# Kernel optimization log

Hardware: AMD Instinct MI355X
Metric: run time of the kernel (lower is better)

## Reference

```python
import jax, jax.numpy as jnp
import numpy as np

N_U = 50000; N_I = 50000; F = 128; H = 128; E = 800000; G = 512; C = 16; L = 3
EPS = 1e-5


def setup_inputs() -> dict:
    key = jax.random.key(0)
    ks = jax.random.split(key, 22)
    s = 1.0 / np.sqrt(H)
    inp = {}
    inp["x_user"] = jax.random.normal(ks[0], (N_U, F), jnp.float32)
    inp["x_item"] = jax.random.normal(ks[1], (N_I, F), jnp.float32)
    inp["edge_u2i"] = jnp.stack([jax.random.randint(ks[2], (E,), 0, N_U),
                                 jax.random.randint(ks[3], (E,), 0, N_I)])
    inp["edge_i2u"] = jnp.stack([jax.random.randint(ks[4], (E,), 0, N_I),
                                 jax.random.randint(ks[5], (E,), 0, N_U)])
    inp["batch_user"] = jnp.sort(jax.random.randint(ks[6], (N_U,), 0, G))
    inp["batch_item"] = jnp.sort(jax.random.randint(ks[7], (N_I,), 0, G))
    # GraphConv params per layer per relation (in-dim == hidden == 128, so stackable)
    inp["Wrel_u2i"] = jax.random.uniform(ks[8], (L, H, F), jnp.float32, -s, s)
    inp["Wroot_u2i"] = jax.random.uniform(ks[9], (L, H, F), jnp.float32, -s, s)
    inp["b_u2i"] = jax.random.uniform(ks[10], (L, H), jnp.float32, -s, s)
    inp["Wrel_i2u"] = jax.random.uniform(ks[11], (L, H, F), jnp.float32, -s, s)
    inp["Wroot_i2u"] = jax.random.uniform(ks[12], (L, H, F), jnp.float32, -s, s)
    inp["b_i2u"] = jax.random.uniform(ks[13], (L, H), jnp.float32, -s, s)
    # BatchNorm (one module per node type, reused across layers)
    inp["bn_g_user"] = jnp.ones((H,), jnp.float32)
    inp["bn_b_user"] = jnp.zeros((H,), jnp.float32)
    inp["bn_g_item"] = jnp.ones((H,), jnp.float32)
    inp["bn_b_item"] = jnp.zeros((H,), jnp.float32)
    # per-layer classifier heads
    inp["fc_W"] = jax.random.uniform(ks[14], (L, C, H), jnp.float32, -s, s)
    inp["fc_b"] = jax.random.uniform(ks[15], (L, C), jnp.float32, -s, s)
    return inp


def _graph_conv(x_src, x_dst, edge, Wrel, Wroot, b, n_dst):
    # GraphConv, aggr='add': W_rel @ sum_{j in N(i)} x_j + W_root @ x_i + b
    agg = jax.ops.segment_sum(x_src[edge[0]], edge[1], num_segments=n_dst)  # [n_dst, F]
    return agg @ Wrel.T + x_dst @ Wroot.T + b


def _bn(x, g, b):
    # BatchNorm1d over nodes, training-mode batch statistics (biased var)
    m = x.mean(0)
    v = jnp.mean((x - m) ** 2, axis=0)
    return (x - m) * jax.lax.rsqrt(v + EPS) * g + b


def reference(x_user, x_item, edge_u2i, edge_i2u, batch_user, batch_item,
              Wrel_u2i, Wroot_u2i, b_u2i, Wrel_i2u, Wroot_i2u, b_i2u,
              bn_g_user, bn_b_user, bn_g_item, bn_b_item, fc_W, fc_b):
    batch_all = jnp.concatenate([batch_user, batch_item])
    cnt = jax.ops.segment_sum(jnp.ones((N_U + N_I,), jnp.float32), batch_all,
                              num_segments=G)
    cnt = jnp.maximum(cnt, 1.0)[:, None]
    feats = []
    xu, xi = x_user, x_item
    for l in range(L):
        new_i = _graph_conv(xu, xi, edge_u2i, Wrel_u2i[l], Wroot_u2i[l], b_u2i[l], N_I)
        new_u = _graph_conv(xi, xu, edge_i2u, Wrel_i2u[l], Wroot_i2u[l], b_i2u[l], N_U)
        xu = _bn(jax.nn.relu(new_u), bn_g_user, bn_b_user)
        xi = _bn(jax.nn.relu(new_i), bn_g_item, bn_b_item)
        pooled = jax.ops.segment_sum(jnp.concatenate([xu, xi], 0), batch_all,
                                     num_segments=G) / cnt  # global mean pool [G, H]
        feats.append(pooled)
    feats = jnp.stack(feats)  # [L, G, H]
    # eval mode: F.dropout is identity; per-layer linear heads
    logits = jnp.einsum('lgh,lch->lgc', feats, fc_W) + fc_b[:, None, :]  # [L, G, C]
    return (logits, feats)
```

## Files before the change

kernel.cpp:

```cpp
#include <hip/hip_runtime.h>

#define NN 50000
#define FD 128
#define NE 800000
#define NG 512
#define NC 16
#define NL 3
#define NTOT 100000
#define NBLK 391
#define NBUCK 196
#define CAP 10240
#define BINTILE 2048
#define NBINBLK 782
#define BNEPS 1e-5f
#define LOGITS_N (NL*NG*NC)

typedef unsigned short u16;
typedef unsigned char u8;
typedef __attribute__((ext_vector_type(8))) short short8;
typedef __attribute__((ext_vector_type(4))) float f32x4;

#define OFF_GCNT     0ul
#define OFF_BCUR     4096ul
#define OFF_ACC      5120ul
#define MEMSET_BYTES 7168ul
#define OFF_USTART   7680ul
#define OFF_ISTART   10240ul
#define OFF_INVCNT   12800ul
#define OFF_BNSC     14848ul
#define OFF_BNSH     15872ul
#define OFF_ROWRANGE 16896ul
#define OFF_WB       817152ul
#define OFF_CSR      1210368ul
#define OFF_N0I      9238528ul
#define OFF_N0U      22038528ul
#define OFF_N1U      34838528ul
#define OFF_N1I      47638528ul
#define OFF_XU0      60438528ul
#define OFF_XI0      73238528ul
#define OFF_WBS      73238528ul
#define OFF_BVEC     73369600ul

static __device__ __forceinline__ float bf2f(u16 v) {
  return __uint_as_float(((unsigned)v) << 16);
}
static __device__ __forceinline__ u16 f2bf(float f) {
  unsigned u = __float_as_uint(f);
  return (u16)((u + 0x7FFFu + ((u >> 16) & 1u)) >> 16);
}
template<int RELU>
static __device__ __forceinline__ void accT8(float* a, int4 v) {
  unsigned w[4] = {(unsigned)v.x, (unsigned)v.y, (unsigned)v.z, (unsigned)v.w};
  #pragma unroll
  for (int i = 0; i < 4; i++) {
    float lo = __uint_as_float(w[i] << 16);
    float hi = __uint_as_float(w[i] & 0xffff0000u);
    if (RELU) { lo = lo > 0.f ? lo : 0.f; hi = hi > 0.f ? hi : 0.f; }
    a[2*i]   += lo;
    a[2*i+1] += hi;
  }
}
static __device__ __forceinline__ void unp8(float* a, int4 v) {
  a[0] = __uint_as_float(((unsigned)v.x) << 16);
  a[1] = __uint_as_float(((unsigned)v.x) & 0xffff0000u);
  a[2] = __uint_as_float(((unsigned)v.y) << 16);
  a[3] = __uint_as_float(((unsigned)v.y) & 0xffff0000u);
  a[4] = __uint_as_float(((unsigned)v.z) << 16);
  a[5] = __uint_as_float(((unsigned)v.z) & 0xffff0000u);
  a[6] = __uint_as_float(((unsigned)v.w) << 16);
  a[7] = __uint_as_float(((unsigned)v.w) & 0xffff0000u);
}
static __device__ __forceinline__ int relu2(int w) {
  int lo = (w & 0x00008000) ? 0 : (w & 0x0000FFFF);
  int hi = (w < 0)          ? 0 : (int)(w & 0xFFFF0000u);
  return lo | hi;
}

__global__ __launch_bounds__(256) void k_hist_batch(const int* __restrict__ bu,
                                                    const int* __restrict__ bi,
                                                    int* __restrict__ gcnt) {
  int i = blockIdx.x*256 + threadIdx.x;
  if (i >= NTOT) return;
  int type = i >= NN;
  int g = type ? bi[i-NN] : bu[i];
  atomicAdd(&gcnt[type*NG + g], 1);
}

__global__ __launch_bounds__(512) void k_scan_g(const int* __restrict__ gcnt,
                                                int* __restrict__ ustart,
                                                int* __restrict__ istart,
                                                float* __restrict__ invcnt) {
  __shared__ int pu[512], pi[512];
  int t = threadIdx.x;
  int cu = gcnt[t], ci = gcnt[NG + t];
  pu[t] = cu; pi[t] = ci;
  __syncthreads();
  for (int off = 1; off < 512; off <<= 1) {
    int vu = (t >= off) ? pu[t-off] : 0;
    int vi = (t >= off) ? pi[t-off] : 0;
    __syncthreads();
    pu[t] += vu; pi[t] += vi;
    __syncthreads();
  }
  ustart[t] = pu[t] - cu;
  istart[t] = pi[t] - ci;
  if (t == 511) { ustart[NG] = pu[511]; istart[NG] = pi[511]; }
  int c = cu + ci;
  invcnt[t] = 1.0f / (float)(c > 0 ? c : 1);
}

__global__ __launch_bounds__(256) void k_bin(const int* __restrict__ eu2i,
                                             const int* __restrict__ ei2u,
                                             int* __restrict__ bcursor,
                                             int* __restrict__ binned) {
  __shared__ int hist[256];
  __shared__ int scan[256];
  __shared__ int gbase[256];
  __shared__ int rbuf[BINTILE];
  __shared__ u8 rbk[BINTILE];
  int tid = threadIdx.x;
  int base = blockIdx.x * BINTILE;
  hist[tid] = 0;
  __syncthreads();
  int packr[8], bkr[8], rankr[8];
  #pragma unroll
  for (int c = 0; c < 8; c++) {
    int idx = base + c*256 + tid;
    if (idx < 2*NE) {
      int rel = idx >= NE;
      int e = rel ? idx - NE : idx;
      const int* edge = rel ? ei2u : eu2i;
      int s = edge[e];
      int d = edge[NE + e];
      int slot = d + (rel ? NN : 0);
      int bk = slot >> 9;
      bkr[c] = bk;
      packr[c] = ((slot & 511) << 17) | s;
      rankr[c] = atomicAdd(&hist[bk], 1);
    } else bkr[c] = -1;
  }
  __syncthreads();
  scan[tid] = hist[tid];
  __syncthreads();
  for (int o = 1; o < 256; o <<= 1) {
    int v = (tid >= o) ? scan[tid - o] : 0;
    __syncthreads();
    scan[tid] += v;
    __syncthreads();
  }
  if (tid < NBUCK && hist[tid] > 0)
    gbase[tid] = atomicAdd(&bcursor[tid], hist[tid]);
  __syncthreads();
  #pragma unroll
  for (int c = 0; c < 8; c++) {
    if (bkr[c] >= 0) {
      int bk = bkr[c];
      int lpos = scan[bk] - hist[bk] + rankr[c];
      rbuf[lpos] = packr[c];
      rbk[lpos] = (u8)bk;
    }
  }
  __syncthreads();
  int nv = min(BINTILE, 2*NE - base);
  for (int j = tid; j < nv; j += 256) {
    int bk = rbk[j];
    int outpos = bk*CAP + gbase[bk] + (j - (scan[bk] - hist[bk]));
    binned[outpos] = rbuf[j];
  }
}

__global__ __launch_bounds__(256) void k_csrbuild(const int* __restrict__ bcursor,
                                                  int* __restrict__ csrbin,
                                                  int2* __restrict__ rowrange) {
  __shared__ int lcnt[512];
  __shared__ int scan2[256];
  __shared__ int lcsr[CAP];
  int b = blockIdx.x;
  int tid = threadIdx.x;
  int slot0 = b << 9;
  int nslots = min(512, NTOT - slot0);
  int n = bcursor[b];
  int gb = b * CAP;
  lcnt[tid] = 0; lcnt[tid + 256] = 0;
  __syncthreads();
  for (int i = tid; i < n; i += 256) {
    int e = csrbin[gb + i];
    atomicAdd(&lcnt[e >> 17], 1);
  }
  __syncthreads();
  int v0 = lcnt[2*tid], v1 = lcnt[2*tid + 1];
  int ps = v0 + v1;
  scan2[tid] = ps;
  __syncthreads();
  for (int o = 1; o < 256; o <<= 1) {
    int v = (tid >= o) ? scan2[tid - o] : 0;
    __syncthreads();
    scan2[tid] += v;
    __syncthreads();
  }
  int e0 = scan2[tid] - ps;
  int e1 = e0 + v0;
  if (2*tid < nslots)     rowrange[slot0 + 2*tid]     = make_int2(gb + e0, gb + e0 + v0);
  if (2*tid + 1 < nslots) rowrange[slot0 + 2*tid + 1] = make_int2(gb + e1, gb + e1 + v1);
  __syncthreads();
  lcnt[2*tid] = e0; lcnt[2*tid + 1] = e1;
  __syncthreads();
  for (int i = tid; i < n; i += 256) {
    int e = csrbin[gb + i];
    int pos = atomicAdd(&lcnt[e >> 17], 1);
    lcsr[pos] = e & 0x1FFFF;
  }
  __syncthreads();
  for (int i = tid; i < n; i += 256) csrbin[gb + i] = lcsr[i];
}

__global__ __launch_bounds__(256) void k_castX(const float* __restrict__ xu,
                                               const float* __restrict__ xi,
                                               u16* __restrict__ xbu,
                                               u16* __restrict__ xbi) {
  int b = blockIdx.x;
  int half = b >= 6250;
  const float* src = half ? xi : xu;
  u16* dst = half ? xbi : xbu;
  int i = ((half ? b - 6250 : b)*256 + threadIdx.x) * 4;
  float4 v = *(const float4*)(src + i);
  ushort4 o = { f2bf(v.x), f2bf(v.y), f2bf(v.z), f2bf(v.w) };
  *(ushort4*)(dst + i) = o;
}

__global__ __launch_bounds__(256) void k_castW(const float* __restrict__ WrelA,
                                               const float* __restrict__ WrootA,
                                               const float* __restrict__ WrelB,
                                               const float* __restrict__ WrootB,
                                               u16* __restrict__ WB) {
  int idx = blockIdx.x*256 + threadIdx.x;
  int lr = idx >> 15;
  int rem = idx & 32767;
  int h = rem >> 8;
  int k = rem & 255;
  int l = lr >> 1;
  int rel = lr & 1;
  const float* Wr = rel ? WrelB : WrelA;
  const float* Wo = rel ? WrootB : WrootA;
  float v = (k < FD) ? Wr[(l*FD + h)*FD + k] : Wo[(l*FD + h)*FD + (k-FD)];
  WB[idx] = f2bf(v);
}

__global__ __launch_bounds__(256) void k_bnfold2(const float* __restrict__ WrelA,
                                                 const float* __restrict__ WrootA,
                                                 const float* __restrict__ WrelB,
                                                 const float* __restrict__ WrootB,
                                                 int l,
                                                 const float* __restrict__ accSQ,
                                                 const float* __restrict__ gu,
                                                 const float* __restrict__ bu_,
                                                 const float* __restrict__ gi,
                                                 const float* __restrict__ bi_,
                                                 u16* __restrict__ WBs,
                                                 float* __restrict__ bvec,
                                                 float* __restrict__ bnsc,
                                                 float* __restrict__ bnsh) {
  __shared__ float sc_l[256], sh_l[256];
  int tid = threadIdx.x;
  {
    int type = tid >> 7;
    int c = tid & 127;
    float s = accSQ[tid];
    float q = accSQ[256 + tid];
    float inv = 1.0f / (float)NN;
    float mean = s * inv;
    float var = q * inv - mean*mean;
    float rstd = rsqrtf(var + BNEPS);
    float g = type ? gi[c] : gu[c];
    float bb = type ? bi_[c] : bu_[c];
    float sc = rstd * g;
    sc_l[tid] = sc;
    sh_l[tid] = bb - mean * sc;
  }
  __syncthreads();
  int b = blockIdx.x;
  int lastb = gridDim.x - 1;
  if (b == lastb) {
    bnsc[tid] = sc_l[tid];
    bnsh[tid] = sh_l[tid];
  } else if (b < 64) {
    int e = b*256 + tid;
    int rel = e >> 13;
    int rem = e & 8191;
    int h = rem >> 6;
    int k0 = (rem & 63) * 4;
    const float* Wr = rel ? WrelB : WrelA;
    const float* Wo = rel ? WrootB : WrootA;
    const float* scs = sc_l + (rel ? 128 : 0);
    const float* scd = sc_l + (rel ? 0 : 128);
    u16 t[4];
    #pragma unroll
    for (int j = 0; j < 4; j++) {
      int k = k0 + j;
      float v = (k < FD) ? Wr[((size_t)l*FD + h)*FD + k] * scs[k]
                         : Wo[((size_t)l*FD + h)*FD + (k - FD)] * scd[k - FD];
      t[j] = f2bf(v);
    }
    ushort4 o = { t[0], t[1], t[2], t[3] };
    *(ushort4*)(WBs + rel*32768 + h*256 + k0) = o;
  } else {
    int vid = (b - 64)*256 + tid;
    int kind = vid >> 8;
    int rel = (vid >> 7) & 1;
    int h = vid & 127;
    const float* W = kind ? (rel ? WrootB : WrootA) : (rel ? WrelB : WrelA);
    const float* sh = sh_l + ((kind ^ rel) ? 128 : 0);
    const float* wrow = W + ((size_t)l*FD + h)*FD;
    float s = 0.f;
    #pragma unroll
    for (int k = 0; k < FD; k += 4) {
      float4 wv = *(const float4*)(wrow + k);
      float4 sv = { sh[k], sh[k+1], sh[k+2], sh[k+3] };
      s += wv.x*sv.x + wv.y*sv.y + wv.z*sv.z + wv.w*sv.w;
    }
    bvec[kind*256 + rel*128 + h] = s;
  }
}

template<int RELU>
__global__ __launch_bounds__(256) void k_gather(const u16* __restrict__ curU,
                                                const u16* __restrict__ curI,
                                                const int2* __restrict__ rowrange,
                                                const int* __restrict__ csr,
                                                u16* __restrict__ aggI,
                                                u16* __restrict__ aggU) {
  int b = blockIdx.x;
  int half = b >= 12500;
  int blk = half ? b - 12500 : b;
  const u16* src = half ? curI : curU;
  u16* out = half ? aggU : aggI;
  int slotbase = half ? NN : 0;
  int wid = __builtin_amdgcn_readfirstlane(threadIdx.x >> 6);
  int row = blk*4 + wid;
  int lane = threadIdx.x & 63;
  int q = lane >> 4;
  int c16 = (lane & 15) * 8;
  const u16* sp = src + c16;
  int2 pr = rowrange[slotbase + row];
  int p = pr.x, pe = pr.y;
  float a0[8], a1[8];
  #pragma unroll
  for (int j = 0; j < 8; j++) { a0[j] = 0.f; a1[j] = 0.f; }
  if (p + 8 <= pe) {
    int i0 = csr[p + q], i1 = csr[p + 4 + q];
    while (p + 16 <= pe) {
      int n0 = csr[p + 8 + q], n1 = csr[p + 12 + q];
      int4 v0 = *(const int4*)(sp + (size_t)i0*FD);
      int4 v1 = *(const int4*)(sp + (size_t)i1*FD);
      accT8<RELU>(a0, v0); accT8<RELU>(a1, v1);
      i0 = n0; i1 = n1; p += 8;
    }
    int4 v0 = *(const int4*)(sp + (size_t)i0*FD);
    int4 v1 = *(const int4*)(sp + (size_t)i1*FD);
    accT8<RELU>(a0, v0); accT8<RELU>(a1, v1);
    p += 8;
  }
  int rem = pe - p;
  if (q < rem) {
    int s = csr[p + q];
    accT8<RELU>(a0, *(const int4*)(sp + (size_t)s*FD));
  }
  if (q + 4 < rem) {
    int s = csr[p + 4 + q];
    accT8<RELU>(a1, *(const int4*)(sp + (size_t)s*FD));
  }
  #pragma unroll
  for (int j = 0; j < 8; j++) a0[j] += a1[j];
  #pragma unroll
  for (int j = 0; j < 8; j++) {
    a0[j] += __shfl_xor(a0[j], 16);
    a0[j] += __shfl_xor(a0[j], 32);
  }
  if (q == 0) {
    int4 o;
    o.x = (unsigned)f2bf(a0[0]) | ((unsigned)f2bf(a0[1]) << 16);
    o.y = (unsigned)f2bf(a0[2]) | ((unsigned)f2bf(a0[3]) << 16);
    o.z = (unsigned)f2bf(a0[4]) | ((unsigned)f2bf(a0[5]) << 16);
    o.w = (unsigned)f2bf(a0[6]) | ((unsigned)f2bf(a0[7]) << 16);
    *(int4*)(out + (size_t)row*FD + c16) = o;
  }
}

__global__ __launch_bounds__(256) void k_gemm(u16* __restrict__ newU,
                                              u16* __restrict__ newI,
                                              const u16* __restrict__ curU,
                                              const u16* __restrict__ curI,
                                              const u16* __restrict__ WBl,
                                              const float* __restrict__ bI2U,
                                              const float* __restrict__ bU2I,
                                              float* __restrict__ accSQ,
                                              const float* __restrict__ bvec,
                                              const int2* __restrict__ rowrange,
                                              int fold) {
  __shared__ u16 smem[128*72*2];
  __shared__ float Sred[2][4][128];
  u16* As = smem;
  u16* Bs = smem + 128*72;
  u16* Cs = smem;
  int ty = blockIdx.y;
  u16* A1 = ty ? newI : newU;
  const u16* A2 = ty ? curI : curU;
  const u16* WBp = ty ? WBl : (WBl + 32768);
  const float* bias = ty ? bU2I : bI2U;
  const float* b1p = bvec + (ty ? 0 : 128);
  const float* b2p = bvec + 256 + (ty ? 0 : 128);
  int slot0 = ty ? 0 : NN;
  int tid = threadIdx.x;
  int n0 = blockIdx.x * 128;
  int w = __builtin_amdgcn_readfirstlane(tid >> 6);
  int lane = tid & 63;
  int l15 = lane & 15;
  int quad = lane >> 4;
  f32x4 acc[2][8];
  #pragma unroll
  for (int tr = 0; tr < 2; tr++)
    #pragma unroll
    for (int tc = 0; tc < 8; tc++)
      acc[tr][tc] = (f32x4){0.f,0.f,0.f,0.f};

  for (int ch = 0; ch < 4; ch++) {
    const u16* Ap = (ch < 2) ? ((const u16*)A1 + ch*64) : (A2 + (ch-2)*64);
    int dorelu = fold && (ch >= 2);
    #pragma unroll
    for (int i = 0; i < 4; i++) {
      int e = i*256 + tid;
      int r = e >> 3, seg = e & 7;
      int4 v = {0,0,0,0};
      int gr = n0 + r;
      if (gr < NN) v = *(const int4*)(Ap + (size_t)gr*FD + seg*8);
      if (dorelu) { v.x = relu2(v.x); v.y = relu2(v.y); v.z = relu2(v.z); v.w = relu2(v.w); }
      *(int4*)&As[r*72 + seg*8] = v;
    }
    #pragma unroll
    for (int i = 0; i < 4; i++) {
      int e = i*256 + tid;
      int r = e >> 3, seg = e & 7;
      int4 v = *(const int4*)(WBp + r*256 + ch*64 + seg*8);
      *(int4*)&Bs[r*72 + seg*8] = v;
    }
    __syncthreads();
    #pragma unroll
    for (int ks = 0; ks < 2; ks++) {
      int kb = ks*32 + quad*8;
      short8 af0 = *(const short8*)&As[(w*32 + l15)*72 + kb];
      short8 af1 = *(const short8*)&As[(w*32 + 16 + l15)*72 + kb];
      short8 bf[8];
      #pragma unroll
      for (int tc = 0; tc < 8; tc++)
        bf[tc] = *(const short8*)&Bs[(tc*16 + l15)*72 + kb];
      #pragma unroll
      for (int tc = 0; tc < 8; tc++) {
        acc[0][tc] = __builtin_amdgcn_mfma_f32_16x16x32_bf16(af0, bf[tc], acc[0][tc], 0, 0, 0);
        acc[1][tc] = __builtin_amdgcn_mfma_f32_16x16x32_bf16(af1, bf[tc], acc[1][tc], 0, 0, 0);
      }
    }
    __syncthreads();
  }
  float sv[8], qv[8], bj[8], b1j[8];
  #pragma unroll
  for (int tc = 0; tc < 8; tc++) {
    int col = tc*16 + l15;
    float base = bias[col];
    if (fold) { base += b2p[col]; b1j[tc] = b1p[col]; } else b1j[tc] = 0.f;
    bj[tc] = base;
    sv[tc] = 0.f; qv[tc] = 0.f;
  }
  float dg[2][4] = {{0.f,0.f,0.f,0.f},{0.f,0.f,0.f,0.f}};
  if (fold) {
    #pragma unroll
    for (int tr = 0; tr < 2; tr++)
      #pragma unroll
      for (int gq = 0; gq < 4; gq++) {
        int r = n0 + w*32 + tr*16 + quad*4 + gq;
        if (r < NN) {
          int2 rr = rowrange[slot0 + r];
          dg[tr][gq] = (float)(rr.y - rr.x);
        }
      }
  }
  #pragma unroll
  for (int tr = 0; tr < 2; tr++) {
    int rl0 = w*32 + tr*16 + quad*4;
    int rbase = n0 + rl0;
    #pragma unroll
    for (int tc = 0; tc < 8; tc++) {
      int col = tc*16 + l15;
      #pragma unroll
      for (int g = 0; g < 4; g++) {
        int r = rbase + g;
        float v = acc[tr][tc][g] + bj[tc] + dg[tr][g]*b1j[tc];
        Cs[(rl0 + g)*132 + col] = f2bf(v);
        if (r < NN) {
          float y = v > 0.f ? v : 0.f;
          sv[tc] += y; qv[tc] += y*y;
        }
      }
    }
  }
  #pragma unroll
  for (int tc = 0; tc < 8; tc++) {
    sv[tc] += __shfl_xor(sv[tc], 16); qv[tc] += __shfl_xor(qv[tc], 16);
    sv[tc] += __shfl_xor(sv[tc], 32); qv[tc] += __shfl_xor(qv[tc], 32);
  }
  if (quad == 0) {
    #pragma unroll
    for (int tc = 0; tc < 8; tc++) {
      Sred[0][w][tc*16 + l15] = sv[tc];
      Sred[1][w][tc*16 + l15] = qv[tc];
    }
  }
  __syncthreads();
  if (tid < 128) {
    float s = Sred[0][0][tid] + Sred[0][1][tid] + Sred[0][2][tid] + Sred[0][3][tid];
    float q = Sred[1][0][tid] + Sred[1][1][tid] + Sred[1][2][tid] + Sred[1][3][tid];
    atomicAdd(&accSQ[ty*128 + tid], s);
    atomicAdd(&accSQ[256 + ty*128 + tid], q);
  }
  int prow = tid >> 4;
  int pc = (tid & 15) * 8;
  #pragma unroll
  for (int j = 0; j < 8; j++) {
    int row = j*16 + prow;
    int gr = n0 + row;
    int4 vv = *(const int4*)&Cs[row*132 + pc];
    if (gr < NN) *(int4*)(A1 + (size_t)gr*FD + pc) = vv;
  }
}

__global__ __launch_bounds__(256) void k_pool(const u16* __restrict__ newU,
                                              const u16* __restrict__ newI,
                                              const int* __restrict__ ustart,
                                              const int* __restrict__ istart,
                                              const float* __restrict__ bnsc,
                                              const float* __restrict__ bnsh,
                                              const float* __restrict__ invcnt,
                                              float* __restrict__ feats,
                                              float* __restrict__ accSQ) {
  __shared__ float red[16][128];
  int tid = threadIdx.x;
  int g = blockIdx.x;
  if (g == 0) { accSQ[tid] = 0.f; accSQ[256 + tid] = 0.f; }
  int rt = tid >> 4;
  int c8 = (tid & 15) * 8;
  float tot[8];
  #pragma unroll
  for (int j = 0; j < 8; j++) tot[j] = 0.f;
  #pragma unroll
  for (int type = 0; type < 2; type++) {
    const u16* in = type ? newI : newU;
    const int* st = type ? istart : ustart;
    int rs = st[g], re = st[g+1];
    float acc[8];
    #pragma unroll
    for (int j = 0; j < 8; j++) acc[j] = 0.f;
    int r = rs + rt;
    for (; r + 16 < re; r += 32) {
      int4 v0 = *(const int4*)(in + (size_t)r*FD + c8);
      int4 v1 = *(const int4*)(in + (size_t)(r+16)*FD + c8);
      float f0[8], f1[8];
      unp8(f0, v0); unp8(f1, v1);
      #pragma unroll
      for (int j = 0; j < 8; j++)
        acc[j] += (f0[j] > 0.f ? f0[j] : 0.f) + (f1[j] > 0.f ? f1[j] : 0.f);
    }
    for (; r < re; r += 16) {
      int4 v0 = *(const int4*)(in + (size_t)r*FD + c8);
      float f0[8];
      unp8(f0, v0);
      #pragma unroll
      for (int j = 0; j < 8; j++) acc[j] += f0[j] > 0.f ? f0[j] : 0.f;
    }
    #pragma unroll
    for (int j = 0; j < 8; j++) tot[j] += acc[j] * bnsc[type*128 + c8 + j];
    if (rt == 0) {
      float cnt = (float)(re - rs);
      #pragma unroll
      for (int j = 0; j < 8; j++) tot[j] += cnt * bnsh[type*128 + c8 + j];
    }
  }
  #pragma unroll
  for (int j = 0; j < 8; j++) red[rt][c8 + j] = tot[j];
  __syncthreads();
  if (tid < 128) {
    float s = 0.f;
    #pragma unroll
    for (int i = 0; i < 16; i++) s += red[i][tid];
    feats[(size_t)g*FD + tid] = s * invcnt[g];
  }
}

__global__ __launch_bounds__(256) void k_heads(const float* __restrict__ feats,
                                               const float* __restrict__ fcW,
                                               const float* __restrict__ fcb,
                                               float* __restrict__ logits) {
  int idx = blockIdx.x*256 + threadIdx.x;
  if (idx >= LOGITS_N) return;
  int l = idx >> 13;
  int rem = idx & 8191;
  int g = rem >> 4;
  int c = rem & 15;
  const float* f = feats + ((size_t)l*NG + g)*FD;
  const float* w = fcW + ((size_t)l*NC + c)*FD;
  float s = 0.f;
  #pragma unroll
  for (int k = 0; k < FD; k += 4) {
    float4 fv = *(const float4*)(f + k);
    float4 wv = *(const float4*)(w + k);
    s += fv.x*wv.x + fv.y*wv.y + fv.z*wv.z + fv.w*wv.w;
  }
  logits[idx] = s + fcb[l*NC + c];
}

extern "C" void kernel_launch(void* const* d_in, const int* in_sizes, int n_in,
                              void* d_out, int out_size, void* d_ws, size_t ws_size,
                              hipStream_t stream) {
  const float* x_user   = (const float*)d_in[0];
  const float* x_item   = (const float*)d_in[1];
  const int*   eu2i     = (const int*)d_in[2];
  const int*   ei2u     = (const int*)d_in[3];
  const int*   bu       = (const int*)d_in[4];
  const int*   bi       = (const int*)d_in[5];
  const float* Wrel_u2i = (const float*)d_in[6];
  const float* Wroot_u2i= (const float*)d_in[7];
  const float* b_u2i    = (const float*)d_in[8];
  const float* Wrel_i2u = (const float*)d_in[9];
  const float* Wroot_i2u= (const float*)d_in[10];
  const float* b_i2u    = (const float*)d_in[11];
  const float* bn_g_user= (const float*)d_in[12];
  const float* bn_b_user= (const float*)d_in[13];
  const float* bn_g_item= (const float*)d_in[14];
  const float* bn_b_item= (const float*)d_in[15];
  const float* fcW      = (const float*)d_in[16];
  const float* fcb      = (const float*)d_in[17];

  char* ws = (char*)d_ws;
  int*   gcnt   = (int*)(ws + OFF_GCNT);
  int*   bcursor= (int*)(ws + OFF_BCUR);
  float* accSQ  = (float*)(ws + OFF_ACC);
  int*   ustart = (int*)(ws + OFF_USTART);
  int*   istart = (int*)(ws + OFF_ISTART);
  float* invcnt = (float*)(ws + OFF_INVCNT);
  float* bnsc   = (float*)(ws + OFF_BNSC);
  float* bnsh   = (float*)(ws + OFF_BNSH);
  int2*  rowrange = (int2*)(ws + OFF_ROWRANGE);
  u16*   WB     = (u16*)(ws + OFF_WB);
  int*   csrbin = (int*)(ws + OFF_CSR);
  u16*   n0I    = (u16*)(ws + OFF_N0I);
  u16*   n0U    = (u16*)(ws + OFF_N0U);
  u16*   n1U    = (u16*)(ws + OFF_N1U);
  u16*   n1I    = (u16*)(ws + OFF_N1I);
  u16*   xu0    = (u16*)(ws + OFF_XU0);
  u16*   xi0    = (u16*)(ws + OFF_XI0);
  u16*   WBs    = (u16*)(ws + OFF_WBS);
  float* bvec   = (float*)(ws + OFF_BVEC);
  float* fout   = (float*)d_out;
  float* featsAll = fout + LOGITS_N;

  hipMemsetAsync(ws, 0, MEMSET_BYTES, stream);
  k_hist_batch<<<NBLK, 256, 0, stream>>>(bu, bi, gcnt);
  k_bin<<<NBINBLK, 256, 0, stream>>>(eu2i, ei2u, bcursor, csrbin);
  k_scan_g<<<1, 512, 0, stream>>>(gcnt, ustart, istart, invcnt);
  k_csrbuild<<<NBUCK, 256, 0, stream>>>(bcursor, csrbin, rowrange);
  k_castX<<<12500, 256, 0, stream>>>(x_user, x_item, xu0, xi0);
  k_castW<<<256, 256, 0, stream>>>(Wrel_u2i, Wroot_u2i, Wrel_i2u, Wroot_i2u, WB);

  k_gather<0><<<25000, 256, 0, stream>>>(xu0, xi0, rowrange, csrbin, n0I, n0U);
  k_gemm<<<dim3(NBLK,2), 256, 0, stream>>>(n0U, n0I, xu0, xi0, WB,
                                           b_i2u, b_u2i, accSQ,
                                           bvec, rowrange, 0);
  k_bnfold2<<<67, 256, 0, stream>>>(Wrel_u2i, Wroot_u2i, Wrel_i2u, Wroot_i2u,
                                    1, accSQ, bn_g_user, bn_b_user,
                                    bn_g_item, bn_b_item, WBs, bvec, bnsc, bnsh);
  k_pool<<<NG, 256, 0, stream>>>(n0U, n0I, ustart, istart, bnsc, bnsh,
                                 invcnt, featsAll, accSQ);

  k_gather<1><<<25000, 256, 0, stream>>>(n0U, n0I, rowrange, csrbin, n1I, n1U);
  k_gemm<<<dim3(NBLK,2), 256, 0, stream>>>(n1U, n1I, n0U, n0I, WBs,
                                           b_i2u + FD, b_u2i + FD, accSQ,
                                           bvec, rowrange, 1);
  k_bnfold2<<<67, 256, 0, stream>>>(Wrel_u2i, Wroot_u2i, Wrel_i2u, Wroot_i2u,
                                    2, accSQ, bn_g_user, bn_b_user,
                                    bn_g_item, bn_b_item, WBs, bvec, bnsc, bnsh);
  k_pool<<<NG, 256, 0, stream>>>(n1U, n1I, ustart, istart, bnsc, bnsh,
                                 invcnt, featsAll + NG*FD, accSQ);

  k_gather<1><<<25000, 256, 0, stream>>>(n1U, n1I, rowrange, csrbin, n0I, n0U);
  k_gemm<<<dim3(NBLK,2), 256, 0, stream>>>(n0U, n0I, n1U, n1I, WBs,
                                           b_i2u + 2*FD, b_u2i + 2*FD, accSQ,
                                           bvec, rowrange, 1);
  k_bnfold2<<<1, 256, 0, stream>>>(Wrel_u2i, Wroot_u2i, Wrel_i2u, Wroot_i2u,
                                   2, accSQ, bn_g_user, bn_b_user,
                                   bn_g_item, bn_b_item, WBs, bvec, bnsc, bnsh);
  k_pool<<<NG, 256, 0, stream>>>(n0U, n0I, ustart, istart, bnsc, bnsh,
                                 invcnt, featsAll + 2*NG*FD, accSQ);

  k_heads<<<96, 256, 0, stream>>>(featsAll, fcW, fcb, fout);
}
```

Measured before the change: 521.9 us.

## Fuse mean pooling into GEMM epilogue and merge preprocessing kernels

Removes the separate k_pool pass that re-read the new node features per graph. The GEMM epilogue now accumulates relu outputs per graph into a float P buffer, using shared-memory atomics for the first six graphs of a tile and global atomics otherwise. k_bnfold2 then applies the BN scale and shift to those pooled sums to produce feats. The cast-X, cast-W and batch-histogram kernels are merged into one k_pre launch, and double-banked stat accumulators replace zeroing in k_pool. The cost is extra atomics in the GEMM epilogue, and the float atomic sums make results order-dependent.

```diff
diff --git a/kernel.cpp b/kernel.cpp
--- a/kernel.cpp
+++ b/kernel.cpp
@@ -23,23 +23,20 @@
 #define OFF_GCNT     0ul
 #define OFF_BCUR     4096ul
 #define OFF_ACC      5120ul
-#define MEMSET_BYTES 7168ul
-#define OFF_USTART   7680ul
-#define OFF_ISTART   10240ul
-#define OFF_INVCNT   12800ul
-#define OFF_BNSC     14848ul
-#define OFF_BNSH     15872ul
+#define MEMSET_BYTES 9216ul
+#define OFF_USTART   9728ul
+#define OFF_ISTART   12288ul
+#define OFF_INVCNT   14848ul
 #define OFF_ROWRANGE 16896ul
 #define OFF_WB       817152ul
 #define OFF_CSR      1210368ul
 #define OFF_N0I      9238528ul
 #define OFF_N0U      22038528ul
-#define OFF_N1U      34838528ul
-#define OFF_N1I      47638528ul
+#define OFF_P        34838528ul
+#define OFF_WBS      35362816ul
+#define OFF_BVEC     35493888ul
 #define OFF_XU0      60438528ul
 #define OFF_XI0      73238528ul
-#define OFF_WBS      73238528ul
-#define OFF_BVEC     73369600ul
 
 static __device__ __forceinline__ float bf2f(u16 v) {
   return __uint_as_float(((unsigned)v) << 16);
@@ -60,30 +57,51 @@
     a[2*i+1] += hi;
   }
 }
-static __device__ __forceinline__ void unp8(float* a, int4 v) {
-  a[0] = __uint_as_float(((unsigned)v.x) << 16);
-  a[1] = __uint_as_float(((unsigned)v.x) & 0xffff0000u);
-  a[2] = __uint_as_float(((unsigned)v.y) << 16);
-  a[3] = __uint_as_float(((unsigned)v.y) & 0xffff0000u);
-  a[4] = __uint_as_float(((unsigned)v.z) << 16);
-  a[5] = __uint_as_float(((unsigned)v.z) & 0xffff0000u);
-  a[6] = __uint_as_float(((unsigned)v.w) << 16);
-  a[7] = __uint_as_float(((unsigned)v.w) & 0xffff0000u);
-}
 static __device__ __forceinline__ int relu2(int w) {
   int lo = (w & 0x00008000) ? 0 : (w & 0x0000FFFF);
   int hi = (w < 0)          ? 0 : (int)(w & 0xFFFF0000u);
   return lo | hi;
 }
 
-__global__ __launch_bounds__(256) void k_hist_batch(const int* __restrict__ bu,
-                                                    const int* __restrict__ bi,
-                                                    int* __restrict__ gcnt) {
-  int i = blockIdx.x*256 + threadIdx.x;
-  if (i >= NTOT) return;
-  int type = i >= NN;
-  int g = type ? bi[i-NN] : bu[i];
-  atomicAdd(&gcnt[type*NG + g], 1);
+__global__ __launch_bounds__(256) void k_pre(const float* __restrict__ xu,
+                                             const float* __restrict__ xi,
+                                             u16* __restrict__ xbu,
+                                             u16* __restrict__ xbi,
+                                             const float* __restrict__ WrelA,
+                                             const float* __restrict__ WrootA,
+                                             const float* __restrict__ WrelB,
+                                             const float* __restrict__ WrootB,
+                                             u16* __restrict__ WB,
+                                             const int* __restrict__ bu,
+                                             const int* __restrict__ bi,
+                                             int* __restrict__ gcnt) {
+  int b = blockIdx.x;
+  if (b < 12500) {
+    int half = b >= 6250;
+    const float* src = half ? xi : xu;
+    u16* dst = half ? xbi : xbu;
+    int i = ((half ? b - 6250 : b)*256 + threadIdx.x) * 4;
+    float4 v = *(const float4*)(src + i);
+    ushort4 o = { f2bf(v.x), f2bf(v.y), f2bf(v.z), f2bf(v.w) };
+    *(ushort4*)(dst + i) = o;
+  } else if (b < 12756) {
+    int idx = (b - 12500)*256 + threadIdx.x;
+    int lr = idx >> 15;
+    int rem = idx & 32767;
+    int h = rem >> 8;
+    int k = rem & 255;
+    int rel = lr & 1;
+    const float* Wr = rel ? WrelB : WrelA;
+    const float* Wo = rel ? WrootB : WrootA;
+    float v = (k < FD) ? Wr[h*FD + k] : Wo[h*FD + (k-FD)];
+    WB[idx] = f2bf(v);
+  } else {
+    int i = (b - 12756)*256 + threadIdx.x;
+    if (i >= NTOT) return;
+    int type = i >= NN;
+    int g = type ? bi[i-NN] : bu[i];
+    atomicAdd(&gcnt[type*NG + g], 1);
+  }
 }
 
 __global__ __launch_bounds__(512) void k_scan_g(const int* __restrict__ gcnt,
@@ -214,52 +232,25 @@
   for (int i = tid; i < n; i += 256) csrbin[gb + i] = lcsr[i];
 }
 
-__global__ __launch_bounds__(256) void k_castX(const float* __restrict__ xu,
-                                               const float* __restrict__ xi,
-                                               u16* __restrict__ xbu,
-                                               u16* __restrict__ xbi) {
-  int b = blockIdx.x;
-  int half = b >= 6250;
-  const float* src = half ? xi : xu;
-  u16* dst = half ? xbi : xbu;
-  int i = ((half ? b - 6250 : b)*256 + threadIdx.x) * 4;
-  float4 v = *(const float4*)(src + i);
-  ushort4 o = { f2bf(v.x), f2bf(v.y), f2bf(v.z), f2bf(v.w) };
-  *(ushort4*)(dst + i) = o;
-}
-
-__global__ __launch_bounds__(256) void k_castW(const float* __restrict__ WrelA,
-                                               const float* __restrict__ WrootA,
-                                               const float* __restrict__ WrelB,
-                                               const float* __restrict__ WrootB,
-                                               u16* __restrict__ WB) {
-  int idx = blockIdx.x*256 + threadIdx.x;
-  int lr = idx >> 15;
-  int rem = idx & 32767;
-  int h = rem >> 8;
-  int k = rem & 255;
-  int l = lr >> 1;
-  int rel = lr & 1;
-  const float* Wr = rel ? WrelB : WrelA;
-  const float* Wo = rel ? WrootB : WrootA;
-  float v = (k < FD) ? Wr[(l*FD + h)*FD + k] : Wo[(l*FD + h)*FD + (k-FD)];
-  WB[idx] = f2bf(v);
-}
-
 __global__ __launch_bounds__(256) void k_bnfold2(const float* __restrict__ WrelA,
                                                  const float* __restrict__ WrootA,
                                                  const float* __restrict__ WrelB,
                                                  const float* __restrict__ WrootB,
                                                  int l,
                                                  const float* __restrict__ accSQ,
+                                                 float* __restrict__ accSQz,
                                                  const float* __restrict__ gu,
                                                  const float* __restrict__ bu_,
-                                                 const float* __restrict__ gi,
+                                                 const float* __restrict__ gi_,
                                                  const float* __restrict__ bi_,
                                                  u16* __restrict__ WBs,
                                                  float* __restrict__ bvec,
-                                                 float* __restrict__ bnsc,
-                                                 float* __restrict__ bnsh) {
+                                                 float* __restrict__ P,
+                                                 const int* __restrict__ ustart,
+                                                 const int* __restrict__ istart,
+                                                 const float* __restrict__ invcnt,
+                                                 float* __restrict__ feats,
+                                                 int mode) {
   __shared__ float sc_l[256], sh_l[256];
   int tid = threadIdx.x;
   {
@@ -271,7 +262,7 @@
     float mean = s * inv;
     float var = q * inv - mean*mean;
     float rstd = rsqrtf(var + BNEPS);
-    float g = type ? gi[c] : gu[c];
+    float g = type ? gi_[c] : gu[c];
     float bb = type ? bi_[c] : bu_[c];
     float sc = rstd * g;
     sc_l[tid] = sc;
@@ -279,46 +270,59 @@
   }
   __syncthreads();
   int b = blockIdx.x;
-  int lastb = gridDim.x - 1;
-  if (b == lastb) {
-    bnsc[tid] = sc_l[tid];
-    bnsh[tid] = sh_l[tid];
-  } else if (b < 64) {
-    int e = b*256 + tid;
-    int rel = e >> 13;
-    int rem = e & 8191;
-    int h = rem >> 6;
-    int k0 = (rem & 63) * 4;
-    const float* Wr = rel ? WrelB : WrelA;
-    const float* Wo = rel ? WrootB : WrootA;
-    const float* scs = sc_l + (rel ? 128 : 0);
-    const float* scd = sc_l + (rel ? 0 : 128);
-    u16 t[4];
-    #pragma unroll
-    for (int j = 0; j < 4; j++) {
-      int k = k0 + j;
-      float v = (k < FD) ? Wr[((size_t)l*FD + h)*FD + k] * scs[k]
-                         : Wo[((size_t)l*FD + h)*FD + (k - FD)] * scd[k - FD];
-      t[j] = f2bf(v);
-    }
-    ushort4 o = { t[0], t[1], t[2], t[3] };
-    *(ushort4*)(WBs + rel*32768 + h*256 + k0) = o;
+  int nfold = mode ? 0 : 66;
+  if (b < nfold) {
+    if (b < 64) {
+      int e = b*256 + tid;
+      int rel = e >> 13;
+      int rem = e & 8191;
+      int h = rem >> 6;
+      int k0 = (rem & 63) * 4;
+      const float* Wr = rel ? WrelB : WrelA;
+      const float* Wo = rel ? WrootB : WrootA;
+      const float* scs = sc_l + (rel ? 128 : 0);
+      const float* scd = sc_l + (rel ? 0 : 128);
+      u16 t[4];
+      #pragma unroll
+      for (int j = 0; j < 4; j++) {
+        int k = k0 + j;
+        float v = (k < FD) ? Wr[((size_t)l*FD + h)*FD + k] * scs[k]
+                           : Wo[((size_t)l*FD + h)*FD + (k - FD)] * scd[k - FD];
+        t[j] = f2bf(v);
+      }
+      ushort4 o = { t[0], t[1], t[2], t[3] };
+      *(ushort4*)(WBs + rel*32768 + h*256 + k0) = o;
+    } else {
+      int vid = (b - 64)*256 + tid;
+      int kind = vid >> 8;
+      int rel = (vid >> 7) & 1;
+      int h = vid & 127;
+      const float* W = kind ? (rel ? WrootB : WrootA) : (rel ? WrelB : WrelA);
+      const float* sh = sh_l + ((kind ^ rel) ? 128 : 0);
+      const float* wrow = W + ((size_t)l*FD + h)*FD;
+      float s = 0.f;
+      #pragma unroll
+      for (int k = 0; k < FD; k += 4) {
+        float4 wv = *(const float4*)(wrow + k);
+        float4 sv = { sh[k], sh[k+1], sh[k+2], sh[k+3] };
+        s += wv.x*sv.x + wv.y*sv.y + wv.z*sv.z + wv.w*sv.w;
+      }
+      bvec[kind*256 + rel*128 + h] = s;
+    }
   } else {
-    int vid = (b - 64)*256 + tid;
-    int kind = vid >> 8;
-    int rel = (vid >> 7) & 1;
-    int h = vid & 127;
-    const float* W = kind ? (rel ? WrootB : WrootA) : (rel ? WrelB : WrelA);
-    const float* sh = sh_l + ((kind ^ rel) ? 128 : 0);
-    const float* wrow = W + ((size_t)l*FD + h)*FD;
-    float s = 0.f;
-    #pragma unroll
-    for (int k = 0; k < FD; k += 4) {
-      float4 wv = *(const float4*)(wrow + k);
-      float4 sv = { sh[k], sh[k+1], sh[k+2], sh[k+3] };
-      s += wv.x*sv.x + wv.y*sv.y + wv.z*sv.z + wv.w*sv.w;
-    }
-    bvec[kind*256 + rel*128 + h] = s;
+    int fb = b - nfold;
+    if (fb == 0) { accSQz[tid] = 0.f; accSQz[256 + tid] = 0.f; }
+    int g = fb*2 + (tid >> 7);
+    int ch = tid & 127;
+    size_t iu = (size_t)g*FD + ch;
+    size_t ii = (size_t)NG*FD + iu;
+    float pu = P[iu];
+    float pi = P[ii];
+    float cu = (float)(ustart[g+1] - ustart[g]);
+    float ci = (float)(istart[g+1] - istart[g]);
+    feats[iu] = invcnt[g] * (sc_l[ch]*pu + cu*sh_l[ch]
+                           + sc_l[128+ch]*pi + ci*sh_l[128+ch]);
+    P[iu] = 0.f; P[ii] = 0.f;
   }
 }
 
@@ -396,12 +400,16 @@
                                               float* __restrict__ accSQ,
                                               const float* __restrict__ bvec,
                                               const int2* __restrict__ rowrange,
+                                              const int* __restrict__ bu,
+                                              const int* __restrict__ bi,
+                                              float* __restrict__ P,
                                               int fold) {
   __shared__ u16 smem[128*72*2];
   __shared__ float Sred[2][4][128];
   u16* As = smem;
   u16* Bs = smem + 128*72;
   u16* Cs = smem;
+  float* Pl = (float*)&smem[16896];
   int ty = blockIdx.y;
   u16* A1 = ty ? newI : newU;
   const u16* A2 = ty ? curI : curU;
@@ -409,6 +417,8 @@
   const float* bias = ty ? bU2I : bI2U;
   const float* b1p = bvec + (ty ? 0 : 128);
   const float* b2p = bvec + 256 + (ty ? 0 : 128);
+  const int* batch = ty ? bi : bu;
+  float* Pg = P + (size_t)ty*NG*FD;
   int slot0 = ty ? 0 : NN;
   int tid = threadIdx.x;
   int n0 = blockIdx.x * 128;
@@ -461,6 +471,11 @@
     }
     __syncthreads();
   }
+  #pragma unroll
+  for (int i = 0; i < 3; i++) Pl[i*256 + tid] = 0.f;
+  __syncthreads();
+
+  int g0 = batch[n0];
   float sv[8], qv[8], bj[8], b1j[8];
   #pragma unroll
   for (int tc = 0; tc < 8; tc++) {
@@ -471,33 +486,37 @@
     sv[tc] = 0.f; qv[tc] = 0.f;
   }
   float dg[2][4] = {{0.f,0.f,0.f,0.f},{0.f,0.f,0.f,0.f}};
-  if (fold) {
-    #pragma unroll
-    for (int tr = 0; tr < 2; tr++)
-      #pragma unroll
-      for (int gq = 0; gq < 4; gq++) {
-        int r = n0 + w*32 + tr*16 + quad*4 + gq;
-        if (r < NN) {
+  int gix[2][4];
+  #pragma unroll
+  for (int tr = 0; tr < 2; tr++)
+    #pragma unroll
+    for (int gq = 0; gq < 4; gq++) {
+      int r = n0 + w*32 + tr*16 + quad*4 + gq;
+      gix[tr][gq] = -1;
+      if (r < NN) {
+        gix[tr][gq] = batch[r] - g0;
+        if (fold) {
           int2 rr = rowrange[slot0 + r];
           dg[tr][gq] = (float)(rr.y - rr.x);
         }
       }
-  }
+    }
   #pragma unroll
   for (int tr = 0; tr < 2; tr++) {
     int rl0 = w*32 + tr*16 + quad*4;
-    int rbase = n0 + rl0;
     #pragma unroll
     for (int tc = 0; tc < 8; tc++) {
       int col = tc*16 + l15;
       #pragma unroll
       for (int g = 0; g < 4; g++) {
-        int r = rbase + g;
         float v = acc[tr][tc][g] + bj[tc] + dg[tr][g]*b1j[tc];
         Cs[(rl0 + g)*132 + col] = f2bf(v);
-        if (r < NN) {
+        int gx = gix[tr][g];
+        if (gx >= 0) {
           float y = v > 0.f ? v : 0.f;
           sv[tc] += y; qv[tc] += y*y;
+          if (gx < 6) atomicAdd(&Pl[gx*128 + col], y);
+          else        atomicAdd(&Pg[(size_t)(g0+gx)*FD + col], y);
         }
       }
     }
@@ -520,6 +539,12 @@
     float q = Sred[1][0][tid] + Sred[1][1][tid] + Sred[1][2][tid] + Sred[1][3][tid];
     atomicAdd(&accSQ[ty*128 + tid], s);
     atomicAdd(&accSQ[256 + ty*128 + tid], q);
+    #pragma unroll
+    for (int gi = 0; gi < 6; gi++) {
+      float pv = Pl[gi*128 + tid];
+      if (pv != 0.f && g0 + gi < NG)
+        atomicAdd(&Pg[(size_t)(g0+gi)*FD + tid], pv);
+    }
   }
   int prow = tid >> 4;
   int pc = (tid & 15) * 8;
@@ -529,68 +554,6 @@
     int gr = n0 + row;
     int4 vv = *(const int4*)&Cs[row*132 + pc];
     if (gr < NN) *(int4*)(A1 + (size_t)gr*FD + pc) = vv;
-  }
-}
-
-__global__ __launch_bounds__(256) void k_pool(const u16* __restrict__ newU,
-                                              const u16* __restrict__ newI,
-                                              const int* __restrict__ ustart,
-                                              const int* __restrict__ istart,
-                                              const float* __restrict__ bnsc,
-                                              const float* __restrict__ bnsh,
-                                              const float* __restrict__ invcnt,
-                                              float* __restrict__ feats,
-                                              float* __restrict__ accSQ) {
-  __shared__ float red[16][128];
-  int tid = threadIdx.x;
-  int g = blockIdx.x;
-  if (g == 0) { accSQ[tid] = 0.f; accSQ[256 + tid] = 0.f; }
-  int rt = tid >> 4;
-  int c8 = (tid & 15) * 8;
-  float tot[8];
-  #pragma unroll
-  for (int j = 0; j < 8; j++) tot[j] = 0.f;
-  #pragma unroll
-  for (int type = 0; type < 2; type++) {
-    const u16* in = type ? newI : newU;
-    const int* st = type ? istart : ustart;
-    int rs = st[g], re = st[g+1];
-    float acc[8];
-    #pragma unroll
-    for (int j = 0; j < 8; j++) acc[j] = 0.f;
-    int r = rs + rt;
-    for (; r + 16 < re; r += 32) {
-      int4 v0 = *(const int4*)(in + (size_t)r*FD + c8);
-      int4 v1 = *(const int4*)(in + (size_t)(r+16)*FD + c8);
-      float f0[8], f1[8];
-      unp8(f0, v0); unp8(f1, v1);
-      #pragma unroll
-      for (int j = 0; j < 8; j++)
-        acc[j] += (f0[j] > 0.f ? f0[j] : 0.f) + (f1[j] > 0.f ? f1[j] : 0.f);
-    }
-    for (; r < re; r += 16) {
-      int4 v0 = *(const int4*)(in + (size_t)r*FD + c8);
-      float f0[8];
-      unp8(f0, v0);
-      #pragma unroll
-      for (int j = 0; j < 8; j++) acc[j] += f0[j] > 0.f ? f0[j] : 0.f;
-    }
-    #pragma unroll
-    for (int j = 0; j < 8; j++) tot[j] += acc[j] * bnsc[type*128 + c8 + j];
-    if (rt == 0) {
-      float cnt = (float)(re - rs);
-      #pragma unroll
-      for (int j = 0; j < 8; j++) tot[j] += cnt * bnsh[type*128 + c8 + j];
-    }
-  }
-  #pragma unroll
-  for (int j = 0; j < 8; j++) red[rt][c8 + j] = tot[j];
-  __syncthreads();
-  if (tid < 128) {
-    float s = 0.f;
-    #pragma unroll
-    for (int i = 0; i < 16; i++) s += red[i][tid];
-    feats[(size_t)g*FD + tid] = s * invcnt[g];
   }
 }
 
@@ -645,59 +608,60 @@
   int*   ustart = (int*)(ws + OFF_USTART);
   int*   istart = (int*)(ws + OFF_ISTART);
   float* invcnt = (float*)(ws + OFF_INVCNT);
-  float* bnsc   = (float*)(ws + OFF_BNSC);
-  float* bnsh   = (float*)(ws + OFF_BNSH);
   int2*  rowrange = (int2*)(ws + OFF_ROWRANGE);
   u16*   WB     = (u16*)(ws + OFF_WB);
   int*   csrbin = (int*)(ws + OFF_CSR);
-  u16*   n0I    = (u16*)(ws + OFF_N0I);
-  u16*   n0U    = (u16*)(ws + OFF_N0U);
-  u16*   n1U    = (u16*)(ws + OFF_N1U);
-  u16*   n1I    = (u16*)(ws + OFF_N1I);
-  u16*   xu0    = (u16*)(ws + OFF_XU0);
-  u16*   xi0    = (u16*)(ws + OFF_XI0);
+  u16*   p0I    = (u16*)(ws + OFF_N0I);
+  u16*   p0U    = (u16*)(ws + OFF_N0U);
+  float* P      = (float*)(ws + OFF_P);
   u16*   WBs    = (u16*)(ws + OFF_WBS);
   float* bvec   = (float*)(ws + OFF_BVEC);
+  u16*   p1U    = (u16*)(ws + OFF_XU0);
+  u16*   p1I    = (u16*)(ws + OFF_XI0);
   float* fout   = (float*)d_out;
   float* featsAll = fout + LOGITS_N;
 
+  float* bank0 = accSQ;
+  float* bank1 = accSQ + 512;
+
   hipMemsetAsync(ws, 0, MEMSET_BYTES, stream);
-  k_hist_batch<<<NBLK, 256, 0, stream>>>(bu, bi, gcnt);
+  hipMemsetAsync(ws + OFF_P, 0, 2ul*NG*FD*4ul, stream);
+  k_pre<<<13147, 256, 0, stream>>>(x_user, x_item, p1U, p1I,
+                                   Wrel_u2i, Wroot_u2i, Wrel_i2u, Wroot_i2u, WB,
+                                   bu, bi, gcnt);
   k_bin<<<NBINBLK, 256, 0, stream>>>(eu2i, ei2u, bcursor, csrbin);
   k_scan_g<<<1, 512, 0, stream>>>(gcnt, ustart, istart, invcnt);
   k_csrbuild<<<NBUCK, 256, 0, stream>>>(bcursor, csrbin, rowrange);
-  k_castX<<<12500, 256, 0, stream>>>(x_user, x_item, xu0, xi0);
-  k_castW<<<256, 256, 0, stream>>>(Wrel_u2i, Wroot_u2i, Wrel_i2u, Wroot_i2u, WB);
-
-  k_gather<0><<<25000, 256, 0, stream>>>(xu0, xi0, rowrange, csrbin, n0I, n0U);
-  k_gemm<<<dim3(NBLK,2), 256, 0, stream>>>(n0U, n0I, xu0, xi0, WB,
-                                           b_i2u, b_u2i, accSQ,
-                                           bvec, rowrange, 0);
-  k_bnfold2<<<67, 256, 0, stream>>>(Wrel_u2i, Wroot_u2i, Wrel_i2u, Wroot_i2u,
-                                    1, accSQ, bn_g_user, bn_b_user,
-                                    bn_g_item, bn_b_item, WBs, bvec, bnsc, bnsh);
-  k_pool<<<NG, 256, 0, stream>>>(n0U, n0I, ustart, istart, bnsc, bnsh,
-                                 invcnt, featsAll, accSQ);
-
-  k_gather<1><<<25000, 256, 0, stream>>>(n0U, n0I, rowrange, csrbin, n1I, n1U);
-  k_gemm<<<dim3(NBLK,2), 256, 0, stream>>>(n1U, n1I, n0U, n0I, WBs,
-                                           b_i2u + FD, b_u2i + FD, accSQ,
-                                           bvec, rowrange, 1);
-  k_bnfold2<<<67, 256, 0, stream>>>(Wrel_u2i, Wroot_u2i, Wrel_i2u, Wroot_i2u,
-                                    2, accSQ, bn_g_user, bn_b_user,
-                                    bn_g_item, bn_b_item, WBs, bvec, bnsc, bnsh);
-  k_pool<<<NG, 256, 0, stream>>>(n1U, n1I, ustart, istart, bnsc, bnsh,
-                                 invcnt, featsAll + NG*FD, accSQ);
-
-  k_gather<1><<<25000, 256, 0, stream>>>(n1U, n1I, rowrange, csrbin, n0I, n0U);
-  k_gemm<<<dim3(NBLK,2), 256, 0, stream>>>(n0U, n0I, n1U, n1I, WBs,
-                                           b_i2u + 2*FD, b_u2i + 2*FD, accSQ,
-                                           bvec, rowrange, 1);
-  k_bnfold2<<<1, 256, 0, stream>>>(Wrel_u2i, Wroot_u2i, Wrel_i2u, Wroot_i2u,
-                                   2, accSQ, bn_g_user, bn_b_user,
-                                   bn_g_item, bn_b_item, WBs, bvec, bnsc, bnsh);
-  k_pool<<<NG, 256, 0, stream>>>(n0U, n0I, ustart, istart, bnsc, bnsh,
-                                 invcnt, featsAll + 2*NG*FD, accSQ);
+
+  k_gather<0><<<25000, 256, 0, stream>>>(p1U, p1I, rowrange, csrbin, p0I, p0U);
+  k_gemm<<<dim3(NBLK,2), 256, 0, stream>>>(p0U, p0I, p1U, p1I, WB,
+                                           b_i2u, b_u2i, bank0,
+                                           bvec, rowrange, bu, bi, P, 0);
+  k_bnfold2<<<322, 256, 0, stream>>>(Wrel_u2i, Wroot_u2i, Wrel_i2u, Wroot_i2u,
+                                     1, bank0, bank1,
+                                     bn_g_user, bn_b_user, bn_g_item, bn_b_item,
+                                     WBs, bvec, P, ustart, istart, invcnt,
+                                     featsAll, 0);
+
+  k_gather<1><<<25000, 256, 0, stream>>>(p0U, p0I, rowrange, csrbin, p1I, p1U);
+  k_gemm<<<dim3(NBLK,2), 256, 0, stream>>>(p1U, p1I, p0U, p0I, WBs,
+                                           b_i2u + FD, b_u2i + FD, bank1,
+                                           bvec, rowrange, bu, bi, P, 1);
+  k_bnfold2<<<322, 256, 0, stream>>>(Wrel_u2i, Wroot_u2i, Wrel_i2u, Wroot_i2u,
+                                     2, bank1, bank0,
+                                     bn_g_user, bn_b_user, bn_g_item, bn_b_item,
+                                     WBs, bvec, P, ustart, istart, invcnt,
+                                     featsAll + NG*FD, 0);
+
+  k_gather<1><<<25000, 256, 0, stream>>>(p1U, p1I, rowrange, csrbin, p0I, p0U);
+  k_gemm<<<dim3(NBLK,2), 256, 0, stream>>>(p0U, p0I, p1U, p1I, WBs,
+                                           b_i2u + 2*FD, b_u2i + 2*FD, bank0,
+                                           bvec, rowrange, bu, bi, P, 1);
+  k_bnfold2<<<256, 256, 0, stream>>>(Wrel_u2i, Wroot_u2i, Wrel_i2u, Wroot_i2u,
+                                     2, bank0, bank1,
+                                     bn_g_user, bn_b_user, bn_g_item, bn_b_item,
+                                     WBs, bvec, P, ustart, istart, invcnt,
+                                     featsAll + 2*NG*FD, 1);
 
   k_heads<<<96, 256, 0, stream>>>(featsAll, fcW, fcb, fout);
 }
```

New measurement: 729.8 us. 1.4x slower.
